# Performance work log

Hardware: AMD Instinct MI355X
Metric: run time of the kernel (lower is better)

## Reference

```python
import jax, jax.numpy as jnp
import numpy as np

B, T, C, H = 16, 4096, 256, 256

def setup_inputs() -> dict:
    key = jax.random.key(0)
    kx, kwi, kbi, kwh, kbh = jax.random.split(key, 5)
    s = 1.0 / np.sqrt(C)
    return {
        "x": jax.random.normal(kx, (B, T, C), dtype=jnp.float32),
        "Wi": jax.random.uniform(kwi, (H, C), dtype=jnp.float32, minval=-s, maxval=s),
        "bi": jax.random.uniform(kbi, (H,), dtype=jnp.float32, minval=-s, maxval=s),
        "Wh": jax.random.uniform(kwh, (H, H), dtype=jnp.float32, minval=-s, maxval=s),
        "bh": jax.random.uniform(kbh, (H,), dtype=jnp.float32, minval=-s, maxval=s),
    }

def reference(x, Wi, bi, Wh, bh):
    # Faithful to the source: Cell computes tanh(i2h(x) + h2h(x)) -- both
    # linears applied to x_t, the hidden state is never consumed, so there
    # is no recurrence and all timesteps can be computed in one fused pass.
    # hidden_states: [B, T, H]
    hidden_states = jnp.tanh(
        jnp.einsum("btc,hc->bth", x, Wi) + bi
        + jnp.einsum("btc,hc->bth", x, Wh) + bh
    )
    h_last = hidden_states[:, -1, :]  # h after the loop
    return (hidden_states, h_last)
```

## Files before the change

### kernel.cpp

```cpp
#include <hip/hip_runtime.h>


using short8 = __attribute__((ext_vector_type(8))) short;
using f32x4  = __attribute__((ext_vector_type(4))) float;

constexpr int Bn = 16, Tn = 4096, Cn = 256, Hn = 256;
constexpr int Mn = Bn * Tn;
constexpr int BM = 32;
constexpr int NBLK = Mn / BM;

__device__ inline unsigned pack2_bf16(float a, float b) {
  unsigned ua = __float_as_uint(a);
  unsigned ub = __float_as_uint(b);
  ua += 0x7fffu + ((ua >> 16) & 1u);
  ub += 0x7fffu + ((ub >> 16) & 1u);
  return (ua >> 16) | (ub & 0xffff0000u);
}

__global__ __launch_bounds__(256) void prep_kernel(
    const float* __restrict__ Wi, const float* __restrict__ bi,
    const float* __restrict__ Wh, const float* __restrict__ bh,
    unsigned short* __restrict__ Wc, float* __restrict__ bc) {
  int idx = blockIdx.x * 256 + threadIdx.x;
  float w = Wi[idx] + Wh[idx];
  unsigned u = __float_as_uint(w);
  u += 0x7fffu + ((u >> 16) & 1u);
  Wc[idx] = (unsigned short)(u >> 16);
  if (blockIdx.x == 0) bc[threadIdx.x] = bi[threadIdx.x] + bh[threadIdx.x];
}

__global__ __launch_bounds__(1024, 8) void gemm_tanh_kernel(
    const float* __restrict__ x, const unsigned short* __restrict__ Wc,
    const float* __restrict__ bc, float* __restrict__ out) {
  __shared__ __align__(16) unsigned short Asm[BM * Cn];

  const int tid  = threadIdx.x;
  const int lane = tid & 63;
  const int wave = tid >> 6;
  const int rid  = lane & 15;
  const int kgrp = lane >> 4;
  const int col  = wave * 16 + rid;
  const int m0   = blockIdx.x * BM;

  const int sr = tid >> 5;
  const int sc = tid & 31;
  const float4* src =
      (const float4*)(x + (size_t)(m0 + sr) * Cn + sc * 8);
  float4 v0 = src[0];
  float4 v1 = src[1];

  short8 bf[8];
#pragma unroll
  for (int ks = 0; ks < 8; ks++)
    bf[ks] = *(const short8*)&Wc[col * Cn + ks * 32 + kgrp * 8];
  const float bias = bc[col];

  {
    uint4 p;
    p.x = pack2_bf16(v0.x, v0.y);
    p.y = pack2_bf16(v0.z, v0.w);
    p.z = pack2_bf16(v1.x, v1.y);
    p.w = pack2_bf16(v1.z, v1.w);
    *(uint4*)&Asm[sr * Cn + ((sc ^ (sr & 7)) << 3)] = p;
  }
  __syncthreads();

  f32x4 acc[2];
  acc[0] = (f32x4)0.f;
  acc[1] = (f32x4)0.f;
#pragma unroll
  for (int ks = 0; ks < 8; ks++) {
#pragma unroll
    for (int mt = 0; mt < 2; mt++) {
      int row = mt * 16 + rid;
      short8 a = *(const short8*)
          &Asm[row * Cn + ((((ks << 2) | kgrp) ^ (rid & 7)) << 3)];
      acc[mt] = __builtin_amdgcn_mfma_f32_16x16x32_bf16(a, bf[ks], acc[mt],
                                                        0, 0, 0);
    }
  }

#pragma unroll
  for (int mt = 0; mt < 2; mt++) {
#pragma unroll
    for (int r = 0; r < 4; r++) {
      int m   = m0 + mt * 16 + kgrp * 4 + r;
      float v = acc[mt][r] + bias;
      float tv = 1.f - 2.f / (__expf(2.f * v) + 1.f);
      out[(size_t)m * Hn + col] = tv;
      if ((m & (Tn - 1)) == (Tn - 1))
        out[(size_t)Mn * Hn + (size_t)(m >> 12) * Hn + col] = tv;
    }
  }
}

extern "C" void kernel_launch(void* const* d_in, const int* in_sizes, int n_in,
                              void* d_out, int out_size, void* d_ws,
                              size_t ws_size, hipStream_t stream) {
  (void)in_sizes; (void)n_in; (void)out_size; (void)ws_size;
  const float* x  = (const float*)d_in[0];
  const float* Wi = (const float*)d_in[1];
  const float* bi = (const float*)d_in[2];
  const float* Wh = (const float*)d_in[3];
  const float* bh = (const float*)d_in[4];
  float* out = (float*)d_out;

  unsigned short* Wc = (unsigned short*)d_ws;
  float* bc = (float*)((char*)d_ws + (size_t)Hn * Cn * sizeof(unsigned short));

  prep_kernel<<<(Hn * Cn) / 256, 256, 0, stream>>>(Wi, bi, Wh, bh, Wc, bc);
  gemm_tanh_kernel<<<NBLK, 1024, 0, stream>>>(x, Wc, bc, out);
}
```

Measured before the change: 142.0 us.

## Keep combined weights resident in LDS and stream x rows with register prefetch

Restructures the GEMM so each of 256 blocks loads the full bf16 weight matrix into swizzled shared memory once and then loops over 256 rows, with each wave streaming its A fragments directly from global memory into registers using a 6-deep prefetch. This removes the repeated per-block weight fetches of the previous 2048-block launch and the LDS staging of x. It trades that for a large shared-memory footprint, which caps occupancy at one block per CU, and for more register pressure from 16 accumulators and the prefetch queue.

After: 131.7 us. 1.08x faster.

```diff
diff --git a/kernel.cpp b/kernel.cpp
--- a/kernel.cpp
+++ b/kernel.cpp
@@ -5,9 +5,11 @@
 using f32x4  = __attribute__((ext_vector_type(4))) float;
 
 constexpr int Bn = 16, Tn = 4096, Cn = 256, Hn = 256;
-constexpr int Mn = Bn * Tn;
-constexpr int BM = 32;
-constexpr int NBLK = Mn / BM;
+constexpr int Mn   = Bn * Tn;
+constexpr int NBLK = 256;
+constexpr int RPB  = Mn / NBLK;
+constexpr int STEPS = 16;
+constexpr int DEPTH = 6;
 
 __device__ inline unsigned pack2_bf16(float a, float b) {
   unsigned ua = __float_as_uint(a);
@@ -29,67 +31,89 @@
   if (blockIdx.x == 0) bc[threadIdx.x] = bi[threadIdx.x] + bh[threadIdx.x];
 }
 
-__global__ __launch_bounds__(1024, 8) void gemm_tanh_kernel(
+__global__ __launch_bounds__(512, 2) void gemm_tanh_kernel(
     const float* __restrict__ x, const unsigned short* __restrict__ Wc,
     const float* __restrict__ bc, float* __restrict__ out) {
-  __shared__ __align__(16) unsigned short Asm[BM * Cn];
+  __shared__ __align__(16) unsigned short Bs[Hn * Cn];
 
   const int tid  = threadIdx.x;
   const int lane = tid & 63;
   const int wave = tid >> 6;
   const int rid  = lane & 15;
   const int kgrp = lane >> 4;
-  const int col  = wave * 16 + rid;
-  const int m0   = blockIdx.x * BM;
+  const int row0 = blockIdx.x * RPB;
 
-  const int sr = tid >> 5;
-  const int sc = tid & 31;
-  const float4* src =
-      (const float4*)(x + (size_t)(m0 + sr) * Cn + sc * 8);
-  float4 v0 = src[0];
-  float4 v1 = src[1];
+  const float* aBase = x + (size_t)(row0 + wave * 16 + rid) * Cn + kgrp * 8;
 
-  short8 bf[8];
+  float4 xq[8][2];
 #pragma unroll
-  for (int ks = 0; ks < 8; ks++)
-    bf[ks] = *(const short8*)&Wc[col * Cn + ks * 32 + kgrp * 8];
-  const float bias = bc[col];
+  for (int s = 0; s < DEPTH; s++) {
+    const float* p = aBase + (s >> 3) * (8 * 16 * Cn) + (s & 7) * 32;
+    xq[s][0] = *(const float4*)p;
+    xq[s][1] = *(const float4*)(p + 4);
+  }
 
-  {
-    uint4 p;
-    p.x = pack2_bf16(v0.x, v0.y);
-    p.y = pack2_bf16(v0.z, v0.w);
-    p.z = pack2_bf16(v1.x, v1.y);
-    p.w = pack2_bf16(v1.z, v1.w);
-    *(uint4*)&Asm[sr * Cn + ((sc ^ (sr & 7)) << 3)] = p;
+  float bias[16];
+#pragma unroll
+  for (int nt = 0; nt < 16; nt++) bias[nt] = bc[nt * 16 + rid];
+
+#pragma unroll
+  for (int i = 0; i < 16; i++) {
+    int g = i * 512 + tid;
+    int n = g >> 5;
+    int c = g & 31;
+    uint4 v = *(const uint4*)(Wc + n * Cn + c * 8);
+    *(uint4*)&Bs[n * Cn + ((c ^ (n & 7)) << 3)] = v;
   }
   __syncthreads();
 
-  f32x4 acc[2];
-  acc[0] = (f32x4)0.f;
-  acc[1] = (f32x4)0.f;
+  f32x4 acc[16];
 #pragma unroll
-  for (int ks = 0; ks < 8; ks++) {
+  for (int nt = 0; nt < 16; nt++) acc[nt] = (f32x4)0.f;
+
 #pragma unroll
-    for (int mt = 0; mt < 2; mt++) {
-      int row = mt * 16 + rid;
-      short8 a = *(const short8*)
-          &Asm[row * Cn + ((((ks << 2) | kgrp) ^ (rid & 7)) << 3)];
-      acc[mt] = __builtin_amdgcn_mfma_f32_16x16x32_bf16(a, bf[ks], acc[mt],
+  for (int s = 0; s < STEPS; s++) {
+    union { unsigned u[4]; short8 v; } cv;
+    float4 a0 = xq[s & 7][0], a1 = xq[s & 7][1];
+    cv.u[0] = pack2_bf16(a0.x, a0.y);
+    cv.u[1] = pack2_bf16(a0.z, a0.w);
+    cv.u[2] = pack2_bf16(a1.x, a1.y);
+    cv.u[3] = pack2_bf16(a1.z, a1.w);
+    short8 af = cv.v;
+
+    if (s + DEPTH < STEPS) {
+      const int s2 = s + DEPTH;
+      const float* p = aBase + (s2 >> 3) * (8 * 16 * Cn) + (s2 & 7) * 32;
+      xq[s2 & 7][0] = *(const float4*)p;
+      xq[s2 & 7][1] = *(const float4*)(p + 4);
+    }
+
+    const int ks = s & 7;
+    const int cs = ((((ks << 2) | kgrp) ^ (rid & 7)) << 3);
+#pragma unroll
+    for (int nt = 0; nt < 16; nt++) {
+      short8 bfr = *(const short8*)&Bs[(nt * 16 + rid) * Cn + cs];
+      acc[nt] = __builtin_amdgcn_mfma_f32_16x16x32_bf16(af, bfr, acc[nt],
                                                         0, 0, 0);
     }
-  }
 
+    if ((s & 7) == 7) {
+      const int j = s >> 3;
+      const int mrow = row0 + (j * 8 + wave) * 16 + kgrp * 4;
 #pragma unroll
-  for (int mt = 0; mt < 2; mt++) {
+      for (int nt = 0; nt < 16; nt++) {
+        const int n = nt * 16 + rid;
 #pragma unroll
-    for (int r = 0; r < 4; r++) {
-      int m   = m0 + mt * 16 + kgrp * 4 + r;
-      float v = acc[mt][r] + bias;
-      float tv = 1.f - 2.f / (__expf(2.f * v) + 1.f);
-      out[(size_t)m * Hn + col] = tv;
-      if ((m & (Tn - 1)) == (Tn - 1))
-        out[(size_t)Mn * Hn + (size_t)(m >> 12) * Hn + col] = tv;
+        for (int r = 0; r < 4; r++) {
+          const int m = mrow + r;
+          float v = acc[nt][r] + bias[nt];
+          float tv = 1.f - 2.f / (__expf(2.f * v) + 1.f);
+          out[(size_t)m * Hn + n] = tv;
+          if ((m & (Tn - 1)) == (Tn - 1))
+            out[(size_t)Mn * Hn + (size_t)(m >> 12) * Hn + n] = tv;
+          acc[nt][r] = 0.f;
+        }
+      }
     }
   }
 }
@@ -109,5 +133,5 @@
   float* bc = (float*)((char*)d_ws + (size_t)Hn * Cn * sizeof(unsigned short));
 
   prep_kernel<<<(Hn * Cn) / 256, 256, 0, stream>>>(Wi, bi, Wh, bh, Wc, bc);
-  gemm_tanh_kernel<<<NBLK, 1024, 0, stream>>>(x, Wc, bc, out);
+  gemm_tanh_kernel<<<NBLK, 512, 0, stream>>>(x, Wc, bc, out);
 }
```
